# Kernel optimization log

Hardware: AMD Instinct MI355X
Metric: run time of the kernel (lower is better)

The kernel has to match this reference:

```python
import jax, jax.numpy as jnp
import numpy as np

EMBED = 128
HEADS = 8
B, S = 2, 2048


def setup_inputs() -> dict:
    key = jax.random.key(0)
    ks = jax.random.split(key, 9)
    scale = 1.0 / np.sqrt(EMBED)
    return {
        "values": jax.random.normal(ks[0], (B, S, EMBED), dtype=jnp.float32),
        "keys": jax.random.normal(ks[1], (B, S, EMBED), dtype=jnp.float32),
        "query": jax.random.normal(ks[2], (B, S, EMBED), dtype=jnp.float32),
        "mask": jax.random.randint(ks[3], (B, 1, S, S), 0, 2, dtype=jnp.int32),
        # torch Linear weights: (out_features, in_features)
        "Wv": jax.random.normal(ks[4], (EMBED * HEADS, EMBED), dtype=jnp.float32) * scale,
        "Wk": jax.random.normal(ks[5], (EMBED * HEADS, EMBED), dtype=jnp.float32) * scale,
        "Wq": jax.random.normal(ks[6], (EMBED * HEADS, EMBED), dtype=jnp.float32) * scale,
        "Wu": jax.random.normal(ks[7], (EMBED, EMBED * HEADS), dtype=jnp.float32) * scale,
        "bu": jax.random.normal(ks[8], (EMBED,), dtype=jnp.float32) * 0.01,
    }


def reference(values, keys, query, mask, Wv, Wk, Wq, Wu, bu):
    n, vl, e = values.shape
    kl = keys.shape[1]
    ql = query.shape[1]
    h = Wv.shape[0] // e

    v = (values @ Wv.T).reshape(n, vl, h, e)   # (n, k, h, d)
    k = (keys @ Wk.T).reshape(n, kl, h, e)
    q = (query @ Wq.T).reshape(n, ql, h, e)

    dot = jnp.einsum("nqhd,nkhd->nhqk", q, k)  # (n, h, q, k)
    dot = jnp.where(mask == 0, jnp.float32(-1e20), dot)
    attn = jax.nn.softmax(dot / jnp.sqrt(jnp.float32(e)), axis=3)

    out = jnp.einsum("nhqk,nkhd->nqhd", attn, v).reshape(n, ql, h * e)
    return out @ Wu.T + bu
```

## Files before the change

### kernel.cpp

```cpp
#include <hip/hip_runtime.h>

typedef unsigned short u16;
typedef unsigned int u32;
typedef unsigned long long u64;
typedef __attribute__((ext_vector_type(8))) short bf16x8;
typedef __attribute__((ext_vector_type(4))) float f32x4;
typedef __attribute__((ext_vector_type(16))) float f32x16;
typedef __attribute__((ext_vector_type(4))) u32 u32x4;
typedef __attribute__((ext_vector_type(4))) int i32x4;
typedef __attribute__((ext_vector_type(4))) u16 u16x4t;

#define GLOAD16(gp, lp)                                                        \
  __builtin_amdgcn_global_load_lds(                                            \
      (__attribute__((address_space(1))) void*)(gp),                           \
      (__attribute__((address_space(3))) void*)(lp), 16, 0, 0)

#if __has_builtin(__builtin_amdgcn_exp2f)
#define EXP2(x) __builtin_amdgcn_exp2f(x)
#else
#define EXP2(x) __expf(0.6931471805599453f * (x))
#endif

#define Z16                                                                    \
  { 0.f, 0.f, 0.f, 0.f, 0.f, 0.f, 0.f, 0.f, 0.f, 0.f, 0.f, 0.f, 0.f, 0.f,     \
    0.f, 0.f }

__device__ __forceinline__ u16 f2bf(float f) {
  u32 u = __builtin_bit_cast(u32, f);
  u += 0x7FFFu + ((u >> 16) & 1u);
  return (u16)(u >> 16);
}

__device__ __forceinline__ float bf2f(short s) {
  return __builtin_bit_cast(float, (u32)(u16)s << 16);
}

__device__ __forceinline__ u32 cvtpk(float lo, float hi) {
  u32 r;
  asm("v_cvt_pk_bf16_f32 %0, %1, %2" : "=v"(r) : "v"(lo), "v"(hi));
  return r;
}

__device__ __forceinline__ void plswap(u32& a, u32& b) {
  asm volatile("v_permlane32_swap_b32 %0, %1" : "+v"(a), "+v"(b));
}

__device__ __forceinline__ f32x4 MFMA(bf16x8 a, bf16x8 b, f32x4 c) {
  return __builtin_amdgcn_mfma_f32_16x16x32_bf16(a, b, c, 0, 0, 0);
}
__device__ __forceinline__ f32x16 MFMA32(bf16x8 a, bf16x8 b, f32x16 c) {
  return __builtin_amdgcn_mfma_f32_32x32x16_bf16(a, b, c, 0, 0, 0);
}

__device__ __forceinline__ u32x4 cvt8(f32x4 a, f32x4 b) {
  u32x4 o;
  o[0] = cvtpk(a[0], a[1]);
  o[1] = cvtpk(a[2], a[3]);
  o[2] = cvtpk(b[0], b[1]);
  o[3] = cvtpk(b[2], b[3]);
  return o;
}

__global__ __launch_bounds__(256) void kproj(
    const float* __restrict__ Xq, const float* __restrict__ Xk,
    const float* __restrict__ Xv, const float* __restrict__ Wqf,
    const float* __restrict__ Wkf, const float* __restrict__ Wvf,
    const int* __restrict__ mask, const float* __restrict__ bu,
    const float* __restrict__ Wuf, u16* __restrict__ Qh, u16* __restrict__ Kh,
    u16* __restrict__ Vt, u64* __restrict__ pm64, u16* __restrict__ Wub16,
    float* __restrict__ outp) {
  const int z = blockIdx.z;
  const int mt = blockIdx.x, nt = blockIdx.y;
  const int tid = threadIdx.x;
  if (z == 3) {
    const int fid = mt + nt * 32;
    const int idx = fid * 256 + tid;
    f32x4 bv = *(const f32x4*)(bu + ((idx * 4) & 127));
    *((f32x4*)outp + idx) = bv;
    if (idx < 32768) {
      f32x4 wv4 = *(const f32x4*)(Wuf + (size_t)idx * 4);
      u16x4t o;
      o[0] = f2bf(wv4[0]); o[1] = f2bf(wv4[1]);
      o[2] = f2bf(wv4[2]); o[3] = f2bf(wv4[3]);
      *(u16x4t*)(Wub16 + (size_t)idx * 4) = o;
    }
#pragma unroll
    for (int j = 0; j < 2; j++) {
      const u32 W = fid * 512 + j * 256 + tid;
      const u32 half = W & 1, q = (W >> 1) & 2047, t5 = (W >> 12) & 31,
                b = W >> 17;
      const int* src =
          mask + ((size_t)b * 2048 + q) * 2048 + t5 * 64 + half * 32;
      i32x4 v[8];
#pragma unroll
      for (int k = 0; k < 8; k++) v[k] = *(const i32x4*)(src + k * 4);
      u32 wbits = 0;
#pragma unroll
      for (int k = 0; k < 8; k++) {
        if (v[k][0]) wbits |= 1u << (k * 4 + 0);
        if (v[k][1]) wbits |= 1u << (k * 4 + 1);
        if (v[k][2]) wbits |= 1u << (k * 4 + 2);
        if (v[k][3]) wbits |= 1u << (k * 4 + 3);
      }
      ((u32*)pm64)[W] = wbits;
    }
    return;
  }
  __shared__ alignas(128) u16 ldsA[128 * 128];
  __shared__ alignas(128) u16 ldsB[64 * 128];
  const float* X = z == 0 ? Xq : (z == 1 ? Xk : Xv);
  const float* W = z == 0 ? Wqf : (z == 1 ? Wkf : Wvf);
  const int w = tid >> 6, lane = tid & 63;
  const int lo = lane & 15, hi = lane >> 4;

#pragma unroll
  for (int i = 0; i < 8; i++) {
    int cid = i * 256 + tid;
    int r = cid >> 4, c = cid & 15;
    const float* src = X + (size_t)(mt * 128 + r) * 128 + c * 8;
    f32x4 a = *(const f32x4*)src;
    f32x4 b = *(const f32x4*)(src + 4);
    *(u32x4*)(ldsA + r * 128 + (c ^ (r & 7)) * 8) = cvt8(a, b);
  }
#pragma unroll
  for (int i = 0; i < 4; i++) {
    int cid = i * 256 + tid;
    int r = cid >> 4, c = cid & 15;
    const float* src = W + (size_t)(nt * 64 + r) * 128 + c * 8;
    f32x4 a = *(const f32x4*)src;
    f32x4 b = *(const f32x4*)(src + 4);
    *(u32x4*)(ldsB + r * 128 + (c ^ (r & 7)) * 8) = cvt8(a, b);
  }
  __syncthreads();

  const int wm = (w >> 1) * 64, wn = (w & 1) * 32;
  f32x4 zero = {0.f, 0.f, 0.f, 0.f};
  f32x4 acc[4][2];
#pragma unroll
  for (int a = 0; a < 4; a++)
#pragma unroll
    for (int b2 = 0; b2 < 2; b2++) acc[a][b2] = zero;

#pragma unroll
  for (int t = 0; t < 4; t++) {
    bf16x8 af[4], bfr[2];
#pragma unroll
    for (int fm = 0; fm < 4; fm++) {
      int r = wm + fm * 16 + lo;
      int ch = (t * 4 + hi) ^ (r & 7);
      af[fm] = *(const bf16x8*)(ldsA + r * 128 + ch * 8);
    }
#pragma unroll
    for (int fn = 0; fn < 2; fn++) {
      int r = wn + fn * 16 + lo;
      int ch = (t * 4 + hi) ^ (r & 7);
      bfr[fn] = *(const bf16x8*)(ldsB + r * 128 + ch * 8);
    }
#pragma unroll
    for (int fm = 0; fm < 4; fm++)
#pragma unroll
      for (int fn = 0; fn < 2; fn++)
        acc[fm][fn] = MFMA(af[fm], bfr[fn], acc[fm][fn]);
  }

  if (z < 2) {
    u16* dst = z == 0 ? Qh : Kh;
    const float scale = z == 0 ? 0.12753103392461437f : 1.0f;
#pragma unroll
    for (int fm = 0; fm < 4; fm++)
#pragma unroll
      for (int fn = 0; fn < 2; fn++) {
        int n = nt * 64 + wn + fn * 16 + lo;
        int h = n >> 7, d = n & 127;
#pragma unroll
        for (int j = 0; j < 4; j++) {
          int m = mt * 128 + wm + fm * 16 + hi * 4 + j;
          int b = m >> 11, s = m & 2047;
          dst[(((size_t)(b * 8 + h) * 2048) + s) * 128 + d] =
              f2bf(acc[fm][fn][j] * scale);
        }
      }
  } else {
#pragma unroll
    for (int fm = 0; fm < 4; fm++)
#pragma unroll
      for (int fn = 0; fn < 2; fn++) {
        int n = nt * 64 + wn + fn * 16 + lo;
        int h = n >> 7, d = n & 127;
        int m0 = mt * 128 + wm + fm * 16 + hi * 4;
        int b = m0 >> 11, s0 = m0 & 2047;
        u16x4t pk4;
#pragma unroll
        for (int j = 0; j < 4; j++) pk4[j] = f2bf(acc[fm][fn][j]);
        *(u16x4t*)(Vt + ((size_t)(b * 8 + h) * 128 + d) * 2048 + s0) = pk4;
      }
  }
}

__global__ __launch_bounds__(256, 2) void kattn(
    const u16* __restrict__ Qh, const u16* __restrict__ Kh,
    const u16* __restrict__ Vt, const u64* __restrict__ pm64,
    u16* __restrict__ OP, float2* __restrict__ ML, int ntiles) {
  __shared__ alignas(128) u16 ldsK[2][64 * 128];
  __shared__ alignas(128) u16 ldsV[2][128 * 64];
  const int bh = blockIdx.x;
  const int half = blockIdx.y;
  const int qblk = blockIdx.z;
  const int b = bh >> 3, h = bh & 7;
  const int ktbase = half * ntiles;
  u16* outO = OP + (size_t)half * 4194304;
  const float CSH = 24.0f;

  const int tid = threadIdx.x, w = tid >> 6, lane = tid & 63;
  const int lo5 = lane & 31, h5 = lane >> 5;
  const int q0w = qblk * 128 + w * 32;
  const int q = q0w + lo5;
  const u16* Qb = Qh + (size_t)bh * 262144;
  const u16* Kb = Kh + (size_t)bh * 262144;
  const u16* Vb = Vt + (size_t)bh * 262144;
  const u64* pmb = pm64 + ((size_t)b << 16);

  int kgo[4], vgo[4], slo[4];
#pragma unroll
  for (int i = 0; i < 4; i++) {
    int off = (w * 4 + i) * 1024 + lane * 16;
    slo[i] = off;
    { int r = off >> 8, c = (off >> 4) & 15, gs = c ^ (r & 7);
      kgo[i] = r * 128 + gs * 8; }
    { int d = off >> 7, c = (off >> 4) & 7, gs = c ^ (d & 7);
      vgo[i] = d * 2048 + gs * 8; }
  }
  int kro[8], vro[4];
#pragma unroll
  for (int ds = 0; ds < 8; ds++)
    kro[ds] = lo5 * 256 + (((ds * 2 + h5) ^ (lo5 & 7)) * 16);
#pragma unroll
  for (int g2 = 0; g2 < 4; g2++)
    vro[g2] = lo5 * 128 + (((g2 * 2 + h5) ^ (lo5 & 7)) * 16);

  bf16x8 vones;
  {
    u32 onesw = (lo5 == 0) ? 0x3F803F80u : 0u;
    u32x4 t = {onesw, onesw, onesw, onesw};
    vones = __builtin_bit_cast(bf16x8, t);
  }

#define STAGE(kt, bb)                                                          \
  do {                                                                         \
    const int k0_ = (kt) * 64;                                                 \
    _Pragma("unroll") for (int i = 0; i < 4; i++)                              \
        GLOAD16(Kb + (size_t)k0_ * 128 + kgo[i],                               \
                (char*)ldsK + (bb) * 16384 + slo[i]);                          \
    _Pragma("unroll") for (int i = 0; i < 4; i++)                              \
        GLOAD16(Vb + k0_ + vgo[i], (char*)ldsV + (bb) * 16384 + slo[i]);       \
  } while (0)

  bf16x8 qb[8];
#pragma unroll
  for (int ds = 0; ds < 8; ds++)
    qb[ds] = *(const bf16x8*)(Qb + (size_t)q * 128 + ds * 16 + h5 * 8);

  asm volatile("" ::: "memory");
  STAGE(ktbase, 0);
  asm volatile("" ::: "memory");

  f32x16 o0 = Z16, o1 = Z16, o2 = Z16, o3 = Z16, o4 = Z16;

  for (int t = 0; t < ntiles; ++t) {
    const int bb = t & 1;
    __builtin_amdgcn_s_barrier();
    u64 mw = pmb[((size_t)(ktbase + t) << 11) + q];
    if (t + 1 < ntiles) {
      STAGE(ktbase + t + 1, bb ^ 1);
      asm volatile("s_waitcnt vmcnt(9)" ::: "memory");
    } else {
      asm volatile("s_waitcnt vmcnt(1)" ::: "memory");
    }
    __builtin_amdgcn_sched_barrier(0);
    __builtin_amdgcn_s_barrier();
    const char* Kt = (const char*)ldsK + bb * 16384;
    const char* Vl = (const char*)ldsV + bb * 16384;

    f32x16 s0v = Z16, s1v = Z16;
    __builtin_amdgcn_s_setprio(1);
#pragma unroll
    for (int ds = 0; ds < 8; ds++) {
      bf16x8 ka0 = *(const bf16x8*)(Kt + kro[ds]);
      bf16x8 ka1 = *(const bf16x8*)(Kt + kro[ds] + 8192);
      s0v = MFMA32(ka0, qb[ds], s0v);
      s1v = MFMA32(ka1, qb[ds], s1v);
    }
    __builtin_amdgcn_s_setprio(0);

    const u32 mw0 = (u32)mw, mw1 = (u32)(mw >> 32);
#pragma unroll
    for (int r = 0; r < 16; r++) {
      const int rowr = (r & 3) + 8 * (r >> 2) + 4 * h5;
      float p0 = EXP2(s0v[r] - CSH);
      float p1 = EXP2(s1v[r] - CSH);
      p0 = ((mw0 >> rowr) & 1u) ? p0 : 0.0f;
      p1 = ((mw1 >> rowr) & 1u) ? p1 : 0.0f;
      s0v[r] = p0;
      s1v[r] = p1;
    }

    bf16x8 pa[4];
#pragma unroll
    for (int kk = 0; kk < 2; kk++)
#pragma unroll
      for (int sl = 0; sl < 2; sl++) {
        const int rb = sl * 8;
        u32 W0, W1, W2, W3;
        if (kk == 0) {
          W0 = cvtpk(s0v[rb + 0], s0v[rb + 1]);
          W1 = cvtpk(s0v[rb + 2], s0v[rb + 3]);
          W2 = cvtpk(s0v[rb + 4], s0v[rb + 5]);
          W3 = cvtpk(s0v[rb + 6], s0v[rb + 7]);
        } else {
          W0 = cvtpk(s1v[rb + 0], s1v[rb + 1]);
          W1 = cvtpk(s1v[rb + 2], s1v[rb + 3]);
          W2 = cvtpk(s1v[rb + 4], s1v[rb + 5]);
          W3 = cvtpk(s1v[rb + 6], s1v[rb + 7]);
        }
        plswap(W0, W2);
        plswap(W1, W3);
        u32x4 tt = {W0, W1, W2, W3};
        pa[kk * 2 + sl] = __builtin_bit_cast(bf16x8, tt);
      }

    __builtin_amdgcn_s_setprio(1);
#pragma unroll
    for (int gsl = 0; gsl < 4; gsl++) {
      bf16x8 vb0 = *(const bf16x8*)(Vl + vro[gsl] + 0 * 4096);
      bf16x8 vb1 = *(const bf16x8*)(Vl + vro[gsl] + 1 * 4096);
      bf16x8 vb2 = *(const bf16x8*)(Vl + vro[gsl] + 2 * 4096);
      bf16x8 vb3 = *(const bf16x8*)(Vl + vro[gsl] + 3 * 4096);
      o0 = MFMA32(pa[gsl], vb0, o0);
      o1 = MFMA32(pa[gsl], vb1, o1);
      o2 = MFMA32(pa[gsl], vb2, o2);
      o3 = MFMA32(pa[gsl], vb3, o3);
      o4 = MFMA32(pa[gsl], vones, o4);
    }
    __builtin_amdgcn_s_setprio(0);
  }
#undef STAGE

  float linv4[16];
#pragma unroll
  for (int r = 0; r < 16; r++) {
    float lr_ = __shfl(o4[r], h5 * 32);
    linv4[r] = lr_ > 0.f ? 1.0f / lr_ : 0.f;
  }
#pragma unroll
  for (int r = 0; r < 16; r++) {
    const int rowr = (r & 3) + 8 * (r >> 2) + 4 * h5;
    const float fr = linv4[r];
    const size_t base =
        ((size_t)(b * 2048 + q0w + rowr)) * 1024 + h * 128 + lo5;
    outO[base + 0] = f2bf(o0[r] * fr);
    outO[base + 32] = f2bf(o1[r] * fr);
    outO[base + 64] = f2bf(o2[r] * fr);
    outO[base + 96] = f2bf(o3[r] * fr);
  }
  if (lo5 == 0) {
#pragma unroll
    for (int r = 0; r < 16; r++) {
      const int rowr = (r & 3) + 8 * (r >> 2) + 4 * h5;
      ML[((size_t)half << 15) + ((size_t)bh << 11) + q0w + rowr] =
          make_float2(CSH, o4[r]);
    }
  }
}

__global__ __launch_bounds__(256) void koutf(
    const u16* __restrict__ OP, const float2* __restrict__ ML,
    const u16* __restrict__ Wub16, float* __restrict__ out, int nsplit) {
  __shared__ alignas(128) u16 ldsA[2][64 * 128];
  __shared__ alignas(128) u16 ldsW[2][128 * 128];
  const int mt = blockIdx.x;
  const int kc = blockIdx.y;
  const int tid = threadIdx.x, w = tid >> 6, lane = tid & 63;
  const int lo = lane & 15, hi = lane >> 4;

#pragma unroll
  for (int ks = 0; ks < 2; ks++) {
    const int k0 = (kc * 2 + ks) * 128;
#pragma unroll
    for (int i = 0; i < 8; i++) {
      int off = (w * 8 + i) * 1024 + lane * 16;
      int r = off >> 8, c = (off >> 4) & 15, g = c ^ (r & 7);
      GLOAD16(Wub16 + (size_t)r * 1024 + k0 + g * 8, (char*)ldsW[ks] + off);
    }
  }
#pragma unroll
  for (int ks = 0; ks < 2; ks++) {
    const int h = kc * 2 + ks;
    const int k0 = h * 128;
#pragma unroll
    for (int i = 0; i < 4; i++) {
      int cid = i * 256 + tid;
      int r = cid >> 4, c = cid & 15;
      int m = mt * 64 + r, b = m >> 11, q = m & 2047;
      size_t off = (size_t)m * 1024 + k0 + c * 8;
      bf16x8 x = *(const bf16x8*)(OP + off);
      u32x4 ow;
      if (nsplit == 2) {
        bf16x8 y = *(const bf16x8*)(OP + 4194304 + off);
        size_t mli = (((size_t)(b << 3) + h) << 11) + q;
        float2 A = ML[mli];
        float2 Bv = ML[32768 + mli];
        float mm = fmaxf(A.x, Bv.x);
        float w1 = A.y * EXP2(A.x - mm);
        float w2 = Bv.y * EXP2(Bv.x - mm);
        float inv = 1.0f / (w1 + w2);
        w1 *= inv;
        w2 *= inv;
        float f[8];
#pragma unroll
        for (int j = 0; j < 8; j++) f[j] = w1 * bf2f(x[j]) + w2 * bf2f(y[j]);
        ow[0] = cvtpk(f[0], f[1]);
        ow[1] = cvtpk(f[2], f[3]);
        ow[2] = cvtpk(f[4], f[5]);
        ow[3] = cvtpk(f[6], f[7]);
      } else {
        ow = __builtin_bit_cast(u32x4, x);
      }
      *(u32x4*)(ldsA[ks] + r * 128 + (c ^ (r & 7)) * 8) = ow;
    }
  }
  __syncthreads();

  f32x4 zero = {0.f, 0.f, 0.f, 0.f};
  f32x4 acc[8];
#pragma unroll
  for (int fn = 0; fn < 8; fn++) acc[fn] = zero;
  __builtin_amdgcn_s_setprio(1);
#pragma unroll
  for (int ks = 0; ks < 2; ks++) {
#pragma unroll
    for (int t = 0; t < 4; t++) {
      int ra = w * 16 + lo, cha = (t * 4 + hi) ^ (ra & 7);
      bf16x8 af = *(const bf16x8*)(ldsA[ks] + ra * 128 + cha * 8);
#pragma unroll
      for (int fn = 0; fn < 8; fn++) {
        int rb = fn * 16 + lo, chb = (t * 4 + hi) ^ (rb & 7);
        bf16x8 bf_ = *(const bf16x8*)(ldsW[ks] + rb * 128 + chb * 8);
        acc[fn] = MFMA(af, bf_, acc[fn]);
      }
    }
  }
  __builtin_amdgcn_s_setprio(0);

#pragma unroll
  for (int fn = 0; fn < 8; fn++) {
    int n = fn * 16 + lo;
#pragma unroll
    for (int j = 0; j < 4; j++) {
      int m = mt * 64 + w * 16 + hi * 4 + j;
      unsafeAtomicAdd(&out[(size_t)m * 128 + n], acc[fn][j]);
    }
  }
}

extern "C" void kernel_launch(void* const* d_in, const int* in_sizes, int n_in,
                              void* d_out, int out_size, void* d_ws,
                              size_t ws_size, hipStream_t stream) {
  const float* values = (const float*)d_in[0];
  const float* keys = (const float*)d_in[1];
  const float* query = (const float*)d_in[2];
  const int* mask = (const int*)d_in[3];
  const float* Wv = (const float*)d_in[4];
  const float* Wk = (const float*)d_in[5];
  const float* Wq = (const float*)d_in[6];
  const float* Wu = (const float*)d_in[7];
  const float* bu = (const float*)d_in[8];

  char* ws = (char*)d_ws;
  u16* QH = (u16*)(ws + 0);
  u16* KH = (u16*)(ws + 8388608);
  u16* VT = (u16*)(ws + 16777216);
  u64* PM64 = (u64*)(ws + 25165824);
  float2* MLb = (float2*)(ws + 26214400);
  u16* WUB16 = (u16*)(ws + 26738688);
  u16* OP = (u16*)(ws + 27262976);

  const size_t base = 27262976;
  int nsplit = (ws_size >= base + 2ull * 8388608) ? 2 : 1;
  int ntiles = 32 / nsplit;

  float* out = (float*)d_out;
  kproj<<<dim3(32, 16, 4), 256, 0, stream>>>(query, keys, values, Wq, Wk, Wv,
                                             mask, bu, Wu, QH, KH, VT, PM64,
                                             WUB16, out);
  kattn<<<dim3(16, nsplit, 16), 256, 0, stream>>>(QH, KH, VT, PM64, OP, MLb,
                                                  ntiles);
  koutf<<<dim3(64, 4), 256, 0, stream>>>(OP, MLb, WUB16, out, nsplit);
}
```

Measured before the change: 80.48 us.

## Split attention KV range four ways and use 512-thread blocks sharing K/V tiles

The attention kernel moves from 256-thread blocks over 128 queries to 512-thread blocks over 256 queries, so each staged K/V tile in LDS is shared by 8 waves and each thread issues half as many async loads. The KV sequence is split into four parts instead of two when workspace allows. The combine kernel merges four partial outputs using the fixed shift constant, dropping the max/exp rescaling. This adds partial-output traffic and combine work in exchange for more parallelism and better K/V reuse. Launch bounds of 512 threads with 4 blocks per CU may force register spilling.

```diff
diff --git a/kernel.cpp b/kernel.cpp
--- a/kernel.cpp
+++ b/kernel.cpp
@@ -197,33 +197,33 @@
   }
 }
 
-__global__ __launch_bounds__(256, 2) void kattn(
+__global__ __launch_bounds__(512, 4) void kattn(
     const u16* __restrict__ Qh, const u16* __restrict__ Kh,
     const u16* __restrict__ Vt, const u64* __restrict__ pm64,
     u16* __restrict__ OP, float2* __restrict__ ML, int ntiles) {
   __shared__ alignas(128) u16 ldsK[2][64 * 128];
   __shared__ alignas(128) u16 ldsV[2][128 * 64];
   const int bh = blockIdx.x;
-  const int half = blockIdx.y;
+  const int quart = blockIdx.y;
   const int qblk = blockIdx.z;
   const int b = bh >> 3, h = bh & 7;
-  const int ktbase = half * ntiles;
-  u16* outO = OP + (size_t)half * 4194304;
+  const int ktbase = quart * ntiles;
+  u16* outO = OP + (size_t)quart * 4194304;
   const float CSH = 24.0f;
 
   const int tid = threadIdx.x, w = tid >> 6, lane = tid & 63;
   const int lo5 = lane & 31, h5 = lane >> 5;
-  const int q0w = qblk * 128 + w * 32;
+  const int q0w = qblk * 256 + w * 32;
   const int q = q0w + lo5;
   const u16* Qb = Qh + (size_t)bh * 262144;
   const u16* Kb = Kh + (size_t)bh * 262144;
   const u16* Vb = Vt + (size_t)bh * 262144;
   const u64* pmb = pm64 + ((size_t)b << 16);
 
-  int kgo[4], vgo[4], slo[4];
-#pragma unroll
-  for (int i = 0; i < 4; i++) {
-    int off = (w * 4 + i) * 1024 + lane * 16;
+  int kgo[2], vgo[2], slo[2];
+#pragma unroll
+  for (int i = 0; i < 2; i++) {
+    int off = (w * 2 + i) * 1024 + lane * 16;
     slo[i] = off;
     { int r = off >> 8, c = (off >> 4) & 15, gs = c ^ (r & 7);
       kgo[i] = r * 128 + gs * 8; }
@@ -248,10 +248,10 @@
 #define STAGE(kt, bb)                                                          \
   do {                                                                         \
     const int k0_ = (kt) * 64;                                                 \
-    _Pragma("unroll") for (int i = 0; i < 4; i++)                              \
+    _Pragma("unroll") for (int i = 0; i < 2; i++)                              \
         GLOAD16(Kb + (size_t)k0_ * 128 + kgo[i],                               \
                 (char*)ldsK + (bb) * 16384 + slo[i]);                          \
-    _Pragma("unroll") for (int i = 0; i < 4; i++)                              \
+    _Pragma("unroll") for (int i = 0; i < 2; i++)                              \
         GLOAD16(Vb + k0_ + vgo[i], (char*)ldsV + (bb) * 16384 + slo[i]);       \
   } while (0)
 
@@ -272,7 +272,7 @@
     u64 mw = pmb[((size_t)(ktbase + t) << 11) + q];
     if (t + 1 < ntiles) {
       STAGE(ktbase + t + 1, bb ^ 1);
-      asm volatile("s_waitcnt vmcnt(9)" ::: "memory");
+      asm volatile("s_waitcnt vmcnt(5)" ::: "memory");
     } else {
       asm volatile("s_waitcnt vmcnt(1)" ::: "memory");
     }
@@ -366,7 +366,7 @@
 #pragma unroll
     for (int r = 0; r < 16; r++) {
       const int rowr = (r & 3) + 8 * (r >> 2) + 4 * h5;
-      ML[((size_t)half << 15) + ((size_t)bh << 11) + q0w + rowr] =
+      ML[((size_t)quart << 15) + ((size_t)bh << 11) + q0w + rowr] =
           make_float2(CSH, o4[r]);
     }
   }
@@ -402,28 +402,45 @@
       int r = cid >> 4, c = cid & 15;
       int m = mt * 64 + r, b = m >> 11, q = m & 2047;
       size_t off = (size_t)m * 1024 + k0 + c * 8;
-      bf16x8 x = *(const bf16x8*)(OP + off);
+      size_t mli = (((size_t)(b << 3) + h) << 11) + q;
       u32x4 ow;
-      if (nsplit == 2) {
-        bf16x8 y = *(const bf16x8*)(OP + 4194304 + off);
-        size_t mli = (((size_t)(b << 3) + h) << 11) + q;
-        float2 A = ML[mli];
-        float2 Bv = ML[32768 + mli];
-        float mm = fmaxf(A.x, Bv.x);
-        float w1 = A.y * EXP2(A.x - mm);
-        float w2 = Bv.y * EXP2(Bv.x - mm);
-        float inv = 1.0f / (w1 + w2);
+      if (nsplit == 4) {
+        float w0 = ML[mli].y, w1 = ML[32768 + mli].y;
+        float w2 = ML[65536 + mli].y, w3 = ML[98304 + mli].y;
+        float tot = (w0 + w1) + (w2 + w3);
+        float inv = tot > 0.f ? 1.0f / tot : 0.f;
+        bf16x8 x0 = *(const bf16x8*)(OP + off);
+        bf16x8 x1 = *(const bf16x8*)(OP + 4194304 + off);
+        bf16x8 x2 = *(const bf16x8*)(OP + 8388608 + off);
+        bf16x8 x3 = *(const bf16x8*)(OP + 12582912 + off);
+        float f[8];
+#pragma unroll
+        for (int j = 0; j < 8; j++)
+          f[j] = (w0 * bf2f(x0[j]) + w1 * bf2f(x1[j]) + w2 * bf2f(x2[j]) +
+                  w3 * bf2f(x3[j])) *
+                 inv;
+        ow[0] = cvtpk(f[0], f[1]);
+        ow[1] = cvtpk(f[2], f[3]);
+        ow[2] = cvtpk(f[4], f[5]);
+        ow[3] = cvtpk(f[6], f[7]);
+      } else if (nsplit == 2) {
+        float w0 = ML[mli].y, w1 = ML[32768 + mli].y;
+        float tot = w0 + w1;
+        float inv = tot > 0.f ? 1.0f / tot : 0.f;
+        w0 *= inv;
         w1 *= inv;
-        w2 *= inv;
+        bf16x8 x0 = *(const bf16x8*)(OP + off);
+        bf16x8 x1 = *(const bf16x8*)(OP + 4194304 + off);
         float f[8];
 #pragma unroll
-        for (int j = 0; j < 8; j++) f[j] = w1 * bf2f(x[j]) + w2 * bf2f(y[j]);
+        for (int j = 0; j < 8; j++) f[j] = w0 * bf2f(x0[j]) + w1 * bf2f(x1[j]);
         ow[0] = cvtpk(f[0], f[1]);
         ow[1] = cvtpk(f[2], f[3]);
         ow[2] = cvtpk(f[4], f[5]);
         ow[3] = cvtpk(f[6], f[7]);
       } else {
-        ow = __builtin_bit_cast(u32x4, x);
+        bf16x8 x0 = *(const bf16x8*)(OP + off);
+        ow = __builtin_bit_cast(u32x4, x0);
       }
       *(u32x4*)(ldsA[ks] + r * 128 + (c ^ (r & 7)) * 8) = ow;
     }
@@ -480,19 +497,20 @@
   u16* KH = (u16*)(ws + 8388608);
   u16* VT = (u16*)(ws + 16777216);
   u64* PM64 = (u64*)(ws + 25165824);
-  float2* MLb = (float2*)(ws + 26214400);
-  u16* WUB16 = (u16*)(ws + 26738688);
-  u16* OP = (u16*)(ws + 27262976);
-
-  const size_t base = 27262976;
-  int nsplit = (ws_size >= base + 2ull * 8388608) ? 2 : 1;
+  u16* WUB16 = (u16*)(ws + 26214400);
+  float2* MLb = (float2*)(ws + 26476544);
+  u16* OP = (u16*)(ws + 27525184);
+
+  const size_t base = 27525184;
+  int nsplit = (ws_size >= base + 4ull * 8388608) ? 4
+             : (ws_size >= base + 2ull * 8388608) ? 2 : 1;
   int ntiles = 32 / nsplit;
 
   float* out = (float*)d_out;
   kproj<<<dim3(32, 16, 4), 256, 0, stream>>>(query, keys, values, Wq, Wk, Wv,
                                              mask, bu, Wu, QH, KH, VT, PM64,
                                              WUB16, out);
-  kattn<<<dim3(16, nsplit, 16), 256, 0, stream>>>(QH, KH, VT, PM64, OP, MLb,
-                                                  ntiles);
+  kattn<<<dim3(16, nsplit, 8), 512, 0, stream>>>(QH, KH, VT, PM64, OP, MLb,
+                                                 ntiles);
   koutf<<<dim3(64, 4), 256, 0, stream>>>(OP, MLb, WUB16, out, nsplit);
 }
```

After: 148.9 us. +85.1%, slower.
